# Kernel tuning notes

Hardware: AMD Instinct MI355X
Metric: run time of the kernel (lower is better)

Reference implementation:

```python
import jax, jax.numpy as jnp
import numpy as np
from jax import lax

BN_EPS = 1e-5

def _conv1d_same(x, w):
    # x: [N, 1, C], w: [1, 1, k] with k odd -> SAME padding along channel axis
    k = w.shape[-1]
    return lax.conv_general_dilated(x, w, window_strides=(1,),
                                    padding=[(k // 2, k // 2)],
                                    dimension_numbers=('NCH', 'OIH', 'NCH'))

def setup_inputs() -> dict:
    key = jax.random.key(0)
    ks = jax.random.split(key, 6)
    B, C, H, W = 4, 64, 64, 64
    kk = 3  # kernel size from in_dim=64: t=int(abs(log2(64)+1)/2)=3 (odd)
    x = jax.random.normal(ks[0], (B, C, H, W), dtype=jnp.float32)
    q_w = jax.random.normal(ks[1], (1, 1, kk), dtype=jnp.float32) * 0.5
    k_w = jax.random.normal(ks[2], (1, 1, kk), dtype=jnp.float32) * 0.5
    v_w = jax.random.normal(ks[3], (C, C), dtype=jnp.float32) * (1.0 / np.sqrt(C))
    v_b = jnp.zeros((C,), dtype=jnp.float32)
    gamma = jax.random.uniform(ks[4], (1,), dtype=jnp.float32, minval=0.5, maxval=1.5)
    bn_w = jnp.ones((C,), dtype=jnp.float32)
    bn_b = jnp.zeros((C,), dtype=jnp.float32)
    return {"x": x, "q_w": q_w, "k_w": k_w, "v_w": v_w, "v_b": v_b,
            "gamma": gamma, "bn_w": bn_w, "bn_b": bn_b}

def reference(x, q_w, k_w, v_w, v_b, gamma, bn_w, bn_b):
    B, C, H, W = x.shape
    N = H * W
    # conv1d Q/K projections over the channel axis, per spatial position
    xp = x.reshape(B, C, N).transpose(0, 2, 1).reshape(B * N, 1, C)
    q = _conv1d_same(xp, q_w).reshape(B, N, C)   # proj_query: [B, HW, C]
    k = _conv1d_same(xp, k_w).reshape(B, N, C)   # proj_key (pre-permute)
    energy = jnp.einsum('bnc,bmc->bnm', q, k)    # [B, HW, HW]
    attn = jax.nn.softmax(energy, axis=-1)
    # 1x1 value conv
    v = jnp.einsum('oc,bchw->bohw', v_w, x) + v_b[None, :, None, None]
    vv = v.reshape(B, C, N)
    # bmm(value, attention^T)
    out = jnp.einsum('bcm,bnm->bcn', vv, attn).reshape(B, C, H, W)
    y = gamma[0] * out
    # BatchNorm2d, training mode (batch statistics, biased variance)
    mean = jnp.mean(y, axis=(0, 2, 3), keepdims=True)
    var = jnp.var(y, axis=(0, 2, 3), keepdims=True)
    y = (y - mean) * lax.rsqrt(var + BN_EPS)
    y = y * bn_w[None, :, None, None] + bn_b[None, :, None, None]
    return y + x
```

## Files before the change

kernel.cpp:

```cpp
#include <hip/hip_runtime.h>
#include <stdint.h>

using f16 = _Float16;

typedef _Float16 f16x8 __attribute__((ext_vector_type(8)));
typedef _Float16 f16x4 __attribute__((ext_vector_type(4)));
typedef float f32x4 __attribute__((ext_vector_type(4)));

#define LOG2E 1.44269504088896340736f

__device__ __forceinline__ f16 f2h(float f) { return (f16)f; }

#if __has_builtin(__builtin_amdgcn_exp2f)
__device__ __forceinline__ float fexp2(float x) { return __builtin_amdgcn_exp2f(x); }
#else
__device__ __forceinline__ float fexp2(float x) { return exp2f(x); }
#endif

typedef __attribute__((address_space(1))) const uint32_t gu32;
typedef __attribute__((address_space(3))) uint32_t lu32;

__device__ __forceinline__ void dma16(const void* g, void* l) {
  __builtin_amdgcn_global_load_lds((gu32*)g, (lu32*)l, 16, 0, 0);
}

__device__ __forceinline__ f16x8 cvt8(const float* p) {
  const float4 a = *(const float4*)p;
  const float4 b = *(const float4*)(p + 4);
  f16x8 r;
  r[0] = (f16)a.x; r[1] = (f16)a.y; r[2] = (f16)a.z; r[3] = (f16)a.w;
  r[4] = (f16)b.x; r[5] = (f16)b.y; r[6] = (f16)b.z; r[7] = (f16)b.w;
  return r;
}


__global__ __launch_bounds__(256, 2) void pam_pre(
    const float* __restrict__ x, const float* __restrict__ qw,
    const float* __restrict__ kw, const float* __restrict__ vw,
    const float* __restrict__ vb,
    f16* __restrict__ qa, f16* __restrict__ ka2, f16* __restrict__ va3,
    float* __restrict__ gz)
{
  __shared__ alignas(16) f16 xt[64 * 72];
  const int tid = threadIdx.x;
  const int b = blockIdx.x >> 6;
  const int n0 = (blockIdx.x & 63) << 6;
  const int lane = tid & 63;
  const int wv = tid >> 6;
  const int quad = lane >> 4, l15 = lane & 15;

  if (blockIdx.x == 0 && tid < 128) gz[tid] = 0.f;

  {
    const int c = tid >> 2;
    const int j0 = (tid & 3) << 4;
    const float* xp = x + ((size_t)(b * 64 + c) << 12) + n0 + j0;
#pragma unroll
    for (int j = 0; j < 4; ++j) {
      const float4 v0 = *(const float4*)(xp + j * 4);
      const int n = j0 + j * 4;
      xt[(n + 0) * 72 + c] = f2h(v0.x);
      xt[(n + 1) * 72 + c] = f2h(v0.y);
      xt[(n + 2) * 72 + c] = f2h(v0.z);
      xt[(n + 3) * 72 + c] = f2h(v0.w);
    }
  }
  __syncthreads();

  const float qw0 = qw[0], qw1 = qw[1], qw2 = qw[2];
  const float kw0 = kw[0], kw1 = kw[1], kw2 = kw[2];
#pragma unroll
  for (int i = 0; i < 2; ++i) {
    const int n = (tid >> 3) + i * 32;
    const int c8 = tid & 7;
    const f16x8 v0 = *(const f16x8*)&xt[n * 72 + c8 * 8];
    const float lm = (c8 > 0) ? (float)xt[n * 72 + c8 * 8 - 1] : 0.f;
    const float rp = (c8 < 7) ? (float)xt[n * 72 + c8 * 8 + 8] : 0.f;
    f16x8 qv8, kv8;
#pragma unroll
    for (int j = 0; j < 8; ++j) {
      const float xm = (j == 0) ? lm : (float)v0[j - 1];
      const float x0 = (float)v0[j];
      const float xp = (j == 7) ? rp : (float)v0[j + 1];
      qv8[j] = f2h((qw0 * xm + qw1 * x0 + qw2 * xp) * LOG2E);
      kv8[j] = f2h(kw0 * xm + kw1 * x0 + kw2 * xp);
    }
    const int nn = n0 + n;
    *(f16x8*)(qa + ((size_t)((b << 12) + nn) << 6) + c8 * 8) = qv8;
    const int np = nn ^ ((((nn >> 3) & 1) << 2) | ((nn >> 4) & 1));
    *(f16x8*)(ka2 + (((size_t)(b * 8 + c8)) << 15) + (np << 3)) = kv8;
  }

  {
    const f16x8 a0 = *(const f16x8*)&xt[(wv * 16 + l15) * 72 + quad * 8];
    const f16x8 a1 = *(const f16x8*)&xt[(wv * 16 + l15) * 72 + quad * 8 + 32];
    const int nb = n0 + wv * 16 + quad * 4;
#pragma unroll
    for (int ct = 0; ct < 4; ++ct) {
      const int co = ct * 16 + l15;
      const f16x8 b0 = cvt8(vw + co * 64 + quad * 8);
      const f16x8 b1 = cvt8(vw + co * 64 + quad * 8 + 32);
      f32x4 z = {0.f, 0.f, 0.f, 0.f};
      z = __builtin_amdgcn_mfma_f32_16x16x32_f16(a0, b0, z, 0, 0, 0);
      z = __builtin_amdgcn_mfma_f32_16x16x32_f16(a1, b1, z, 0, 0, 0);
      const float vbv = vb[co];
      f16x4 pv;
#pragma unroll
      for (int r = 0; r < 4; ++r) pv[r] = f2h(z[r] + vbv);
      *(f16x4*)(va3 + (((size_t)(b * 512 + (nb >> 3))) << 9)
                + (co << 3) + (nb & 7)) = pv;
    }
  }
}

__global__ __launch_bounds__(512, 2) void pam_attn(
    const f16* __restrict__ qa, const f16* __restrict__ ka2,
    const f16* __restrict__ va3, const float* __restrict__ gam,
    float* __restrict__ y0, float* __restrict__ gs1, float* __restrict__ gs2)
{
  __shared__ alignas(16) f16 kbuf[2][8192];
  __shared__ alignas(16) f16 vbuf[2][8192];
  __shared__ float ldsO[32 * 65];
  __shared__ float ldsM[4][32], ldsL[4][32], ldsMg[32], ldsInv[32];

  const int tid = threadIdx.x;
  const int wv = tid >> 6, lane = tid & 63;
  const int quad = lane >> 4, l15 = lane & 15;
  const int ks = wv & 3, qh = wv >> 2;
  const int b = blockIdx.x & 3;
  const int qb = blockIdx.x >> 2;
  const int qb0 = qb << 5;
  const int phase = qb & 31;

  for (int i = tid; i < 32 * 65; i += 512) ldsO[i] = 0.f;

  const int bn = b << 12;
  f16x8 bq0, bq1;
  {
    const int q = qb0 + qh * 16 + l15;
    const f16* qp = qa + ((size_t)(bn + q) << 6) + quad * 8;
    bq0 = *(const f16x8*)qp;
    bq1 = *(const f16x8*)(qp + 32);
  }

  const f16* kg0 = ka2 + (((size_t)(b * 8 + wv)) << 15) + (lane << 3);
  const f16* vg0 = va3 + ((size_t)b << 18) + (wv << 10) + (lane << 3);

  f32x4 o[4] = {};
  float m = -1e30f, lp = 0.f;

  dma16(kg0 + ((size_t)phase << 10),       kbuf[0] + (wv << 10));
  dma16(kg0 + ((size_t)phase << 10) + 512, kbuf[0] + (wv << 10) + 512);
  dma16(vg0 + ((size_t)phase << 13),       vbuf[0] + (wv << 10));
  dma16(vg0 + ((size_t)phase << 13) + 512, vbuf[0] + (wv << 10) + 512);
  __syncthreads();

  const int u = l15 >> 2;
  const int xmsk = ((u & 1) << 2) | (u >> 1);
  const int pos0 = (ks << 5) + (u << 3) + (l15 & 3);
  const int koff0 = (pos0 ^ xmsk) << 3;
  const int koff1 = koff0 ^ 32;
  const int vbase = ((ks * 4 + quad) << 9) + (l15 << 3);

#pragma unroll 1
  for (int kt = 0; kt < 32; ++kt) {
    const int cur = kt & 1;
    {
      const int tn = (kt + 1 + phase) & 31;
      f16* kd = kbuf[cur ^ 1] + (wv << 10);
      f16* vd = vbuf[cur ^ 1] + (wv << 10);
      dma16(kg0 + ((size_t)tn << 10),       kd);
      dma16(kg0 + ((size_t)tn << 10) + 512, kd + 512);
      dma16(vg0 + ((size_t)tn << 13),       vd);
      dma16(vg0 + ((size_t)tn << 13) + 512, vd + 512);
    }

    const f16* kc = kbuf[cur];
    const f16* vc = vbuf[cur];
    const f16x8 ak00 = *(const f16x8*)(kc + (quad << 10) + koff0);
    const f16x8 ak01 = *(const f16x8*)(kc + ((4 + quad) << 10) + koff0);
    const f16x8 ak10 = *(const f16x8*)(kc + (quad << 10) + koff1);
    const f16x8 ak11 = *(const f16x8*)(kc + ((4 + quad) << 10) + koff1);

    f32x4 z0, z1;
    {
      f32x4 z = {0.f, 0.f, 0.f, 0.f};
      z = __builtin_amdgcn_mfma_f32_16x16x32_f16(ak00, bq0, z, 0, 0, 0);
      z0 = __builtin_amdgcn_mfma_f32_16x16x32_f16(ak01, bq1, z, 0, 0, 0);
    }
    {
      f32x4 z = {0.f, 0.f, 0.f, 0.f};
      z = __builtin_amdgcn_mfma_f32_16x16x32_f16(ak10, bq0, z, 0, 0, 0);
      z1 = __builtin_amdgcn_mfma_f32_16x16x32_f16(ak11, bq1, z, 0, 0, 0);
    }

    float tmax = fmaxf(fmaxf(fmaxf(z0[0], z0[1]), fmaxf(z0[2], z0[3])),
                       fmaxf(fmaxf(z1[0], z1[1]), fmaxf(z1[2], z1[3])));
    tmax = fmaxf(tmax, __shfl_xor(tmax, 16, 64));
    tmax = fmaxf(tmax, __shfl_xor(tmax, 32, 64));
    const bool need = !__all(tmax <= m + 8.f);
    const float mn = need ? fmaxf(m, tmax) : m;

    const float p0 = fexp2(z0[0] - mn);
    const float p1 = fexp2(z0[1] - mn);
    const float p2 = fexp2(z0[2] - mn);
    const float p3 = fexp2(z0[3] - mn);
    const float p4 = fexp2(z1[0] - mn);
    const float p5 = fexp2(z1[1] - mn);
    const float p6 = fexp2(z1[2] - mn);
    const float p7 = fexp2(z1[3] - mn);
    const float ts = ((p0 + p1) + (p2 + p3)) + ((p4 + p5) + (p6 + p7));

    f16x8 pa;
    pa[0] = f2h(p0); pa[1] = f2h(p1); pa[2] = f2h(p2); pa[3] = f2h(p3);
    pa[4] = f2h(p4); pa[5] = f2h(p5); pa[6] = f2h(p6); pa[7] = f2h(p7);

    if (need) {
      const float al = fexp2(m - mn);
      lp = lp * al + ts;
      m = mn;
#pragma unroll
      for (int ct = 0; ct < 4; ++ct)
        for (int r = 0; r < 4; ++r) o[ct][r] *= al;
    } else {
      lp += ts;
    }

#pragma unroll
    for (int ct = 0; ct < 4; ++ct) {
      const f16x8 av = *(const f16x8*)(vc + vbase + ct * 128);
      o[ct] = __builtin_amdgcn_mfma_f32_16x16x32_f16(av, pa, o[ct], 0, 0, 0);
    }
    __syncthreads();
  }

  {
    float v = lp;
    v += __shfl_xor(v, 16, 64);
    v += __shfl_xor(v, 32, 64);
    if (quad == 0) {
      ldsM[ks][qh * 16 + l15] = m;
      ldsL[ks][qh * 16 + l15] = v;
    }
  }
  __syncthreads();

  if (tid < 32) {
    const float M = fmaxf(fmaxf(ldsM[0][tid], ldsM[1][tid]),
                          fmaxf(ldsM[2][tid], ldsM[3][tid]));
    const float lt = ldsL[0][tid] * fexp2(ldsM[0][tid] - M) +
                     ldsL[1][tid] * fexp2(ldsM[1][tid] - M) +
                     ldsL[2][tid] * fexp2(ldsM[2][tid] - M) +
                     ldsL[3][tid] * fexp2(ldsM[3][tid] - M);
    ldsMg[tid] = M;
    ldsInv[tid] = 1.f / lt;
  }
  __syncthreads();

  {
    const int q = qh * 16 + l15;
    const float sc = fexp2(m - ldsMg[q]);
#pragma unroll
    for (int ct = 0; ct < 4; ++ct)
      for (int r = 0; r < 4; ++r)
        atomicAdd(&ldsO[q * 65 + ct * 16 + quad * 4 + r], o[ct][r] * sc);
  }
  __syncthreads();

  const float g = gam[0];
  {
    const int c = tid >> 3;
    const int q0 = (tid & 7) << 2;
    float4 v4;
    float* vp = &v4.x;
    float s1 = 0.f, s2 = 0.f;
    for (int r = 0; r < 4; ++r) {
      const float val = g * ldsO[(q0 + r) * 65 + c] * ldsInv[q0 + r];
      vp[r] = val; s1 += val; s2 += val * val;
    }
    *(float4*)(y0 + ((size_t)(b * 64 + c) << 12) + qb0 + q0) = v4;
    s1 += __shfl_xor(s1, 1, 64);
    s2 += __shfl_xor(s2, 1, 64);
    s1 += __shfl_xor(s1, 2, 64);
    s2 += __shfl_xor(s2, 2, 64);
    s1 += __shfl_xor(s1, 4, 64);
    s2 += __shfl_xor(s2, 4, 64);
    if ((tid & 7) == 0) {
      atomicAdd(&gs1[c], s1);
      atomicAdd(&gs2[c], s2);
    }
  }
}

__global__ __launch_bounds__(256, 2) void pam_apply(
    const float* __restrict__ y0, const float* __restrict__ x,
    const float* __restrict__ gs1, const float* __restrict__ gs2,
    const float* __restrict__ bnw, const float* __restrict__ bnb,
    float* __restrict__ out)
{
  const int i = (blockIdx.x * 256 + threadIdx.x) << 2;
  const int c = (i >> 12) & 63;
  const float inv_n = 1.f / 16384.f;
  const float mean = gs1[c] * inv_n;
  const float var = fmaxf(gs2[c] * inv_n - mean * mean, 0.f);
  const float sc = bnw[c] * rsqrtf(var + 1e-5f);
  const float sh = bnb[c] - mean * sc;
  const float4 y = *(const float4*)(y0 + i);
  const float4 xv = *(const float4*)(x + i);
  float4 r;
  r.x = y.x * sc + sh + xv.x;
  r.y = y.y * sc + sh + xv.y;
  r.z = y.z * sc + sh + xv.z;
  r.w = y.w * sc + sh + xv.w;
  *(float4*)(out + i) = r;
}

extern "C" void kernel_launch(void* const* d_in, const int* in_sizes, int n_in,
                              void* d_out, int out_size, void* d_ws, size_t ws_size,
                              hipStream_t stream)
{
  (void)in_sizes; (void)n_in; (void)out_size; (void)ws_size;
  const float* x   = (const float*)d_in[0];
  const float* qw  = (const float*)d_in[1];
  const float* kw  = (const float*)d_in[2];
  const float* vw  = (const float*)d_in[3];
  const float* vb  = (const float*)d_in[4];
  const float* gam = (const float*)d_in[5];
  const float* bnw = (const float*)d_in[6];
  const float* bnb = (const float*)d_in[7];

  char* ws = (char*)d_ws;
  f16*   qa  = (f16*)(ws);
  f16*   ka2 = (f16*)(ws + (2u << 20));
  f16*   va3 = (f16*)(ws + (4u << 20));
  float* y0  = (float*)(ws + (6u << 20));
  float* gs1 = (float*)(ws + (10u << 20));
  float* gs2 = (float*)(ws + (10u << 20) + 256);

  pam_pre  <<<256, 256, 0, stream>>>(x, qw, kw, vw, vb, qa, ka2, va3, gs1);
  pam_attn <<<512, 512, 0, stream>>>(qa, ka2, va3, gam, y0, gs1, gs2);
  pam_apply<<<1024, 256, 0, stream>>>(y0, x, gs1, gs2, bnw, bnb, (float*)d_out);
}
```

Before: 147.2 us.

## Load V fragments directly from global and shrink preprocessing tiles

The attention kernel no longer stages V tiles through double-buffered LDS. Each lane now loads its four V fragments straight from global memory at the top of every iteration, which halves LDS use and allows a higher occupancy hint in launch bounds. The preprocessing kernel now processes 16 positions per block instead of 64 and launches four times as many blocks to spread work across more CUs. The direct global V loads depend on L2/cache hit rates and add load latency inside the loop, and only half the pre threads do the conv projections.

```diff
diff --git a/kernel.cpp b/kernel.cpp
--- a/kernel.cpp
+++ b/kernel.cpp
@@ -41,10 +41,10 @@
     f16* __restrict__ qa, f16* __restrict__ ka2, f16* __restrict__ va3,
     float* __restrict__ gz)
 {
-  __shared__ alignas(16) f16 xt[64 * 72];
+  __shared__ alignas(16) f16 xt[16 * 72];
   const int tid = threadIdx.x;
-  const int b = blockIdx.x >> 6;
-  const int n0 = (blockIdx.x & 63) << 6;
+  const int b = blockIdx.x >> 8;
+  const int n0 = (blockIdx.x & 255) << 4;
   const int lane = tid & 63;
   const int wv = tid >> 6;
   const int quad = lane >> 4, l15 = lane & 15;
@@ -53,25 +53,19 @@
 
   {
     const int c = tid >> 2;
-    const int j0 = (tid & 3) << 4;
-    const float* xp = x + ((size_t)(b * 64 + c) << 12) + n0 + j0;
-#pragma unroll
-    for (int j = 0; j < 4; ++j) {
-      const float4 v0 = *(const float4*)(xp + j * 4);
-      const int n = j0 + j * 4;
-      xt[(n + 0) * 72 + c] = f2h(v0.x);
-      xt[(n + 1) * 72 + c] = f2h(v0.y);
-      xt[(n + 2) * 72 + c] = f2h(v0.z);
-      xt[(n + 3) * 72 + c] = f2h(v0.w);
-    }
-  }
-  __syncthreads();
-
-  const float qw0 = qw[0], qw1 = qw[1], qw2 = qw[2];
-  const float kw0 = kw[0], kw1 = kw[1], kw2 = kw[2];
-#pragma unroll
-  for (int i = 0; i < 2; ++i) {
-    const int n = (tid >> 3) + i * 32;
+    const int j0 = (tid & 3) << 2;
+    const float4 v0 = *(const float4*)(x + ((size_t)(b * 64 + c) << 12) + n0 + j0);
+    xt[(j0 + 0) * 72 + c] = f2h(v0.x);
+    xt[(j0 + 1) * 72 + c] = f2h(v0.y);
+    xt[(j0 + 2) * 72 + c] = f2h(v0.z);
+    xt[(j0 + 3) * 72 + c] = f2h(v0.w);
+  }
+  __syncthreads();
+
+  if (tid < 128) {
+    const float qw0 = qw[0], qw1 = qw[1], qw2 = qw[2];
+    const float kw0 = kw[0], kw1 = kw[1], kw2 = kw[2];
+    const int n = tid >> 3;
     const int c8 = tid & 7;
     const f16x8 v0 = *(const f16x8*)&xt[n * 72 + c8 * 8];
     const float lm = (c8 > 0) ? (float)xt[n * 72 + c8 * 8 - 1] : 0.f;
@@ -92,34 +86,30 @@
   }
 
   {
-    const f16x8 a0 = *(const f16x8*)&xt[(wv * 16 + l15) * 72 + quad * 8];
-    const f16x8 a1 = *(const f16x8*)&xt[(wv * 16 + l15) * 72 + quad * 8 + 32];
-    const int nb = n0 + wv * 16 + quad * 4;
+    const f16x8 a0 = *(const f16x8*)&xt[l15 * 72 + quad * 8];
+    const f16x8 a1 = *(const f16x8*)&xt[l15 * 72 + quad * 8 + 32];
+    const int co = wv * 16 + l15;
+    const f16x8 b0 = cvt8(vw + co * 64 + quad * 8);
+    const f16x8 b1 = cvt8(vw + co * 64 + quad * 8 + 32);
+    f32x4 z = {0.f, 0.f, 0.f, 0.f};
+    z = __builtin_amdgcn_mfma_f32_16x16x32_f16(a0, b0, z, 0, 0, 0);
+    z = __builtin_amdgcn_mfma_f32_16x16x32_f16(a1, b1, z, 0, 0, 0);
+    const float vbv = vb[co];
+    f16x4 pv;
 #pragma unroll
-    for (int ct = 0; ct < 4; ++ct) {
-      const int co = ct * 16 + l15;
-      const f16x8 b0 = cvt8(vw + co * 64 + quad * 8);
-      const f16x8 b1 = cvt8(vw + co * 64 + quad * 8 + 32);
-      f32x4 z = {0.f, 0.f, 0.f, 0.f};
-      z = __builtin_amdgcn_mfma_f32_16x16x32_f16(a0, b0, z, 0, 0, 0);
-      z = __builtin_amdgcn_mfma_f32_16x16x32_f16(a1, b1, z, 0, 0, 0);
-      const float vbv = vb[co];
-      f16x4 pv;
-#pragma unroll
-      for (int r = 0; r < 4; ++r) pv[r] = f2h(z[r] + vbv);
-      *(f16x4*)(va3 + (((size_t)(b * 512 + (nb >> 3))) << 9)
-                + (co << 3) + (nb & 7)) = pv;
-    }
-  }
-}
-
-__global__ __launch_bounds__(512, 2) void pam_attn(
+    for (int r = 0; r < 4; ++r) pv[r] = f2h(z[r] + vbv);
+    const int nb = n0 + quad * 4;
+    *(f16x4*)(va3 + (((size_t)(b * 512 + (nb >> 3))) << 9)
+              + (co << 3) + (nb & 7)) = pv;
+  }
+}
+
+__global__ __launch_bounds__(512, 6) void pam_attn(
     const f16* __restrict__ qa, const f16* __restrict__ ka2,
     const f16* __restrict__ va3, const float* __restrict__ gam,
     float* __restrict__ y0, float* __restrict__ gs1, float* __restrict__ gs2)
 {
   __shared__ alignas(16) f16 kbuf[2][8192];
-  __shared__ alignas(16) f16 vbuf[2][8192];
   __shared__ float ldsO[32 * 65];
   __shared__ float ldsM[4][32], ldsL[4][32], ldsMg[32], ldsInv[32];
 
@@ -144,15 +134,13 @@
   }
 
   const f16* kg0 = ka2 + (((size_t)(b * 8 + wv)) << 15) + (lane << 3);
-  const f16* vg0 = va3 + ((size_t)b << 18) + (wv << 10) + (lane << 3);
+  const f16* vgp = va3 + ((size_t)b << 18) + ((ks * 4 + quad) << 9) + (l15 << 3);
 
   f32x4 o[4] = {};
   float m = -1e30f, lp = 0.f;
 
   dma16(kg0 + ((size_t)phase << 10),       kbuf[0] + (wv << 10));
   dma16(kg0 + ((size_t)phase << 10) + 512, kbuf[0] + (wv << 10) + 512);
-  dma16(vg0 + ((size_t)phase << 13),       vbuf[0] + (wv << 10));
-  dma16(vg0 + ((size_t)phase << 13) + 512, vbuf[0] + (wv << 10) + 512);
   __syncthreads();
 
   const int u = l15 >> 2;
@@ -160,23 +148,26 @@
   const int pos0 = (ks << 5) + (u << 3) + (l15 & 3);
   const int koff0 = (pos0 ^ xmsk) << 3;
   const int koff1 = koff0 ^ 32;
-  const int vbase = ((ks * 4 + quad) << 9) + (l15 << 3);
 
 #pragma unroll 1
   for (int kt = 0; kt < 32; ++kt) {
     const int cur = kt & 1;
+    const int gcur = (kt + phase) & 31;
+
+    const f16* vt = vgp + ((size_t)gcur << 13);
+    const f16x8 av0 = *(const f16x8*)(vt);
+    const f16x8 av1 = *(const f16x8*)(vt + 128);
+    const f16x8 av2 = *(const f16x8*)(vt + 256);
+    const f16x8 av3 = *(const f16x8*)(vt + 384);
+
     {
       const int tn = (kt + 1 + phase) & 31;
       f16* kd = kbuf[cur ^ 1] + (wv << 10);
-      f16* vd = vbuf[cur ^ 1] + (wv << 10);
       dma16(kg0 + ((size_t)tn << 10),       kd);
       dma16(kg0 + ((size_t)tn << 10) + 512, kd + 512);
-      dma16(vg0 + ((size_t)tn << 13),       vd);
-      dma16(vg0 + ((size_t)tn << 13) + 512, vd + 512);
     }
 
     const f16* kc = kbuf[cur];
-    const f16* vc = vbuf[cur];
     const f16x8 ak00 = *(const f16x8*)(kc + (quad << 10) + koff0);
     const f16x8 ak01 = *(const f16x8*)(kc + ((4 + quad) << 10) + koff0);
     const f16x8 ak10 = *(const f16x8*)(kc + (quad << 10) + koff1);
@@ -226,11 +217,10 @@
       lp += ts;
     }
 
-#pragma unroll
-    for (int ct = 0; ct < 4; ++ct) {
-      const f16x8 av = *(const f16x8*)(vc + vbase + ct * 128);
-      o[ct] = __builtin_amdgcn_mfma_f32_16x16x32_f16(av, pa, o[ct], 0, 0, 0);
-    }
+    o[0] = __builtin_amdgcn_mfma_f32_16x16x32_f16(av0, pa, o[0], 0, 0, 0);
+    o[1] = __builtin_amdgcn_mfma_f32_16x16x32_f16(av1, pa, o[1], 0, 0, 0);
+    o[2] = __builtin_amdgcn_mfma_f32_16x16x32_f16(av2, pa, o[2], 0, 0, 0);
+    o[3] = __builtin_amdgcn_mfma_f32_16x16x32_f16(av3, pa, o[3], 0, 0, 0);
     __syncthreads();
   }
 
@@ -337,7 +327,7 @@
   float* gs1 = (float*)(ws + (10u << 20));
   float* gs2 = (float*)(ws + (10u << 20) + 256);
 
-  pam_pre  <<<256, 256, 0, stream>>>(x, qw, kw, vw, vb, qa, ka2, va3, gs1);
+  pam_pre  <<<1024, 256, 0, stream>>>(x, qw, kw, vw, vb, qa, ka2, va3, gs1);
   pam_attn <<<512, 512, 0, stream>>>(qa, ka2, va3, gam, y0, gs1, gs2);
   pam_apply<<<1024, 256, 0, stream>>>(y0, x, gs1, gs2, bnw, bnb, (float*)d_out);
 }
```

Result: no change. 147.0 us (-0.1%).
